# Performance work log

Hardware: AMD Instinct MI355X
Metric: run time of the kernel (lower is better)

## Reference

```python
import jax, jax.numpy as jnp
import numpy as np

TOKEN_SIZE = 4
NEIGHBOR_SIZE = 3


def setup_inputs() -> dict:
    key = jax.random.key(0)
    ks = jax.random.split(key, 8)
    B, C, H, W = 8, 256, 64, 64
    return {
        "blue_feat": jax.random.normal(ks[0], (B, C, H, W), jnp.float32),
        "white_feat": jax.random.normal(ks[1], (B, C, H, W), jnp.float32),
        "Wq": jax.random.normal(ks[2], (C, C), jnp.float32) * 0.05,
        "bq": jax.random.normal(ks[3], (C,), jnp.float32) * 0.05,
        "Wk": jax.random.normal(ks[4], (C, C), jnp.float32) * 0.05,
        "bk": jax.random.normal(ks[5], (C,), jnp.float32) * 0.05,
        "Wv": jax.random.normal(ks[6], (C, C), jnp.float32) * 0.05,
        "bv": jax.random.normal(ks[7], (C,), jnp.float32) * 0.05,
    }


def _tokens(x, nh, nw, ts):
    # [B,C,H,W] -> [B,nh,nw,C,ts*ts]
    B, C = x.shape[0], x.shape[1]
    return (x.reshape(B, C, nh, ts, nw, ts)
             .transpose(0, 2, 4, 1, 3, 5)
             .reshape(B, nh, nw, C, ts * ts))


def reference(blue_feat, white_feat, Wq, bq, Wk, bk, Wv, bv):
    ts, ns = TOKEN_SIZE, NEIGHBOR_SIZE
    pad = ns // 2
    B, C, H, W = blue_feat.shape
    scale = float((ts * ts) ** -0.5)

    # 1x1 conv projections (pointwise channel mix + bias)
    Q = jnp.einsum('bchw,oc->bohw', blue_feat, Wq) + bq[None, :, None, None]
    K = jnp.einsum('bchw,oc->bohw', white_feat, Wk) + bk[None, :, None, None]
    V = jnp.einsum('bchw,oc->bohw', white_feat, Wv) + bv[None, :, None, None]

    nh, nw = H // ts, W // ts  # H,W divisible by ts -> no padding branch
    Qt = _tokens(Q, nh, nw, ts)  # [B,nh,nw,C,D]
    Kt = _tokens(K, nh, nw, ts)
    Vt = _tokens(V, nh, nw, ts)

    # zero-padded token grid, gather 3x3 neighbor tokens (F.unfold equivalent)
    padw = ((0, 0), (pad, pad), (pad, pad), (0, 0), (0, 0))
    Kp = jnp.pad(Kt, padw)
    Vp = jnp.pad(Vt, padw)
    Knb = jnp.stack([Kp[:, di:di + nh, dj:dj + nw]
                     for di in range(ns) for dj in range(ns)], axis=3)  # [B,nh,nw,9,C,D]
    Vnb = jnp.stack([Vp[:, di:di + nh, dj:dj + nw]
                     for di in range(ns) for dj in range(ns)], axis=3)

    # per-channel attention over neighbor tokens
    attn = jax.nn.softmax(
        jnp.einsum('bhwcd,bhwncd->bhwcn', Qt, Knb) * scale, axis=-1)
    out = jnp.einsum('bhwcn,bhwncd->bhwcd', attn, Vnb)  # [B,nh,nw,C,D]

    enhanced = (out.reshape(B, nh, nw, C, ts, ts)
                   .transpose(0, 3, 1, 4, 2, 5)
                   .reshape(B, C, H, W))
    return blue_feat + enhanced  # out_proj is Identity since c1 == c2
```

## Files before the change

kernel.cpp:

```cpp
#include <hip/hip_runtime.h>
#include <hip/hip_bf16.h>
#include <stdint.h>

typedef float  f32x4  __attribute__((ext_vector_type(4)));
typedef float  f32x2  __attribute__((ext_vector_type(2)));
typedef __bf16 bf16x8 __attribute__((ext_vector_type(8)));

#define LROW 40

__global__ __launch_bounds__(256) void wprep_kernel(
    const float* __restrict__ Wq, const float* __restrict__ Wk,
    const float* __restrict__ Wv, __bf16* __restrict__ Wbf)
{
  const int b = blockIdx.x;
  const int t = b >> 5;
  const float* src = (t == 0) ? Wq : (t == 1) ? Wk : Wv;
  const int off = (b & 31) * 2048 + threadIdx.x * 8;
  f32x4 v0 = *(const f32x4*)(src + off);
  f32x4 v1 = *(const f32x4*)(src + off + 4);
  bf16x8 r;
#pragma unroll
  for (int q = 0; q < 4; ++q) { r[q] = (__bf16)v0[q]; r[q + 4] = (__bf16)v1[q]; }
  *(bf16x8*)(Wbf + t * 65536 + off) = r;
}


__global__ __launch_bounds__(256, 3) void proj_gemm3_kernel(
    const float* __restrict__ blue, const float* __restrict__ white,
    const __bf16* __restrict__ Wbf,
    const float* __restrict__ bq, const float* __restrict__ bk,
    const float* __restrict__ bv,
    __bf16* __restrict__ Qt, __bf16* __restrict__ Kt, __bf16* __restrict__ Vt)
{
  __shared__ __bf16 Bs[2][128 * LROW];

  const int bidhw = blockIdx.x;
  const int lid   = (bidhw & 7) * 192 + (bidhw >> 3);
  const int nb    = lid / 6;
  const int bt    = lid % 6;
  const int tensor = (bt < 4) ? 1 + (bt & 1) : 0;
  const int ob     = (bt < 4) ? (bt >> 1) : (bt & 1);

  const float* X    = (tensor == 0) ? blue : white;
  const float* bias = (tensor == 0) ? bq : (tensor == 1) ? bk : bv;
  __bf16*      Out  = (tensor == 0) ? Qt : (tensor == 1) ? Kt : Vt;
  const __bf16* Wp  = Wbf + tensor * 65536 + ob * (128 * 256);

  const int tid  = threadIdx.x;
  const int lane = tid & 63;
  const int wave = tid >> 6;
  const int wo   = wave >> 1;
  const int wn   = wave & 1;

  const int o0    = ob * 128;
  const int n0    = nb * 128;
  const int batch = n0 >> 12;
  const int p0    = n0 & 4095;
  const int tk0   = p0 >> 4;
  const int trow  = tk0 >> 4;
  const int tcol0 = tk0 & 15;
  const float* Xb = X + (size_t)batch * (256 * 4096);

  const int n2   = tid & 63;
  const int ko   = tid >> 6;
  const int nloc = 2 * n2;
  const int tl   = nloc >> 4;
  const int d    = nloc & 15;
  const int hw   = (trow * 4 + (d >> 2)) * 64 + (tcol0 + tl) * 4 + (d & 3);
  const float* srcB0 = Xb + (size_t)(ko * 8) * 4096 + hw;

  const int lrow = lane & 15;
  const int lk   = (lane >> 4) * 8;
  const int aoff = (wo * 64 + lrow) * 256 + lk;

  f32x4 acc[4][4];
#pragma unroll
  for (int i = 0; i < 4; ++i)
#pragma unroll
    for (int j = 0; j < 4; ++j) acc[i][j] = (f32x4)0.0f;

  f32x2 preA[8], preB[8];

#define LOADB(P, kk) { const float* s_ = srcB0 + (size_t)(kk) * 32 * 4096;          \
    P[0] = *(const f32x2*)(s_);         P[1] = *(const f32x2*)(s_ + 4096);          \
    P[2] = *(const f32x2*)(s_ + 8192);  P[3] = *(const f32x2*)(s_ + 12288);         \
    P[4] = *(const f32x2*)(s_ + 16384); P[5] = *(const f32x2*)(s_ + 20480);         \
    P[6] = *(const f32x2*)(s_ + 24576); P[7] = *(const f32x2*)(s_ + 28672); }

#define STEP(P, kk, BUF) {                                                          \
    bf16x8 r0, r1;                                                                  \
    _Pragma("unroll")                                                               \
    for (int t = 0; t < 8; ++t) { r0[t] = (__bf16)P[t][0]; r1[t] = (__bf16)P[t][1]; } \
    *(bf16x8*)(&Bs[BUF][0] + (nloc + 0) * LROW + ko * 8) = r0;                      \
    *(bf16x8*)(&Bs[BUF][0] + (nloc + 1) * LROW + ko * 8) = r1;                      \
    bf16x8 af[4];                                                                   \
    _Pragma("unroll")                                                               \
    for (int i = 0; i < 4; ++i)                                                     \
      af[i] = *(const bf16x8*)(Wp + aoff + i * 4096 + (kk) * 32);                   \
    if ((kk) + 2 < 8) LOADB(P, (kk) + 2);                                           \
    asm volatile("s_waitcnt lgkmcnt(0)" ::: "memory");                              \
    __builtin_amdgcn_s_barrier();                                                   \
    asm volatile("" ::: "memory");                                                  \
    bf16x8 bfrag[4];                                                                \
    _Pragma("unroll")                                                               \
    for (int j = 0; j < 4; ++j)                                                     \
      bfrag[j] = *(const bf16x8*)(&Bs[BUF][0] + (wn * 64 + j * 16 + lrow) * LROW + lk); \
    _Pragma("unroll")                                                               \
    for (int i = 0; i < 4; ++i)                                                     \
      _Pragma("unroll")                                                             \
      for (int j = 0; j < 4; ++j)                                                   \
        acc[i][j] = __builtin_amdgcn_mfma_f32_16x16x32_bf16(af[i], bfrag[j], acc[i][j], 0, 0, 0); \
  }

  LOADB(preA, 0);
  LOADB(preB, 1);

#pragma unroll
  for (int kp = 0; kp < 4; ++kp) {
    STEP(preA, 2 * kp,     0);
    STEP(preB, 2 * kp + 1, 1);
  }
#undef STEP
#undef LOADB

#pragma unroll
  for (int i = 0; i < 4; ++i) {
    const int obase = o0 + wo * 64 + i * 16 + (lane >> 4) * 4;
#pragma unroll
    for (int j = 0; j < 4; ++j) {
      const int n  = n0 + wn * 64 + j * 16 + (lane & 15);
      const int bb = n >> 12;
      const int pp = n & 4095;
      const int tt = pp >> 4;
      const int tii = tt >> 4;
      const int tjj = tt & 15;
      const int dd  = pp & 15;
      const size_t base = ((size_t)(bb * 16 + tii) * 256) * 256 + tjj * 16 + dd;
#pragma unroll
      for (int r = 0; r < 4; ++r) {
        const int o = obase + r;
        const float v = acc[i][j][r] + bias[o];
        Out[base + (size_t)o * 256] = (__bf16)v;
      }
    }
  }
}

__global__ __launch_bounds__(256) void proj_gemm_kernel(
    const float* __restrict__ blue, const float* __restrict__ white,
    const float* __restrict__ Wq, const float* __restrict__ bq,
    const float* __restrict__ Wk, const float* __restrict__ bk,
    const float* __restrict__ Wv, const float* __restrict__ bv,
    __bf16* __restrict__ Qt, __bf16* __restrict__ Kt, __bf16* __restrict__ Vt)
{
  __shared__ __bf16 As[128 * LROW];
  __shared__ __bf16 Bs[128 * LROW];

  const int bidhw = blockIdx.x;
  const int lid   = (bidhw & 7) * 192 + (bidhw >> 3);
  const int nb    = lid / 6;
  const int bt    = lid % 6;
  const int tensor = (bt < 4) ? 1 + (bt & 1) : 0;
  const int ob     = (bt < 4) ? (bt >> 1) : (bt & 1);

  const float* X    = (tensor == 0) ? blue : white;
  const float* W    = (tensor == 0) ? Wq : (tensor == 1) ? Wk : Wv;
  const float* bias = (tensor == 0) ? bq : (tensor == 1) ? bk : bv;
  __bf16*      Out  = (tensor == 0) ? Qt : (tensor == 1) ? Kt : Vt;

  const int tid  = threadIdx.x;
  const int lane = tid & 63;
  const int wave = tid >> 6;
  const int wo   = wave >> 1;
  const int wn   = wave & 1;

  const int o0 = ob * 128;
  const int n0 = nb * 128;
  const int batch = n0 >> 12;
  const int p0    = n0 & 4095;
  const int tk0   = p0 >> 4;
  const int trow  = tk0 >> 4;
  const int tcol0 = tk0 & 15;
  const float* Xb = X + (size_t)batch * (256 * 4096);

  f32x4 acc[4][4];
#pragma unroll
  for (int i = 0; i < 4; ++i)
#pragma unroll
    for (int j = 0; j < 4; ++j) acc[i][j] = (f32x4)0.0f;

  const int arow  = tid >> 1;
  const int ahalf = tid & 1;
  const int n2   = tid & 63;
  const int ko   = tid >> 6;
  const int nloc = 2 * n2;
  const int tl   = nloc >> 4;
  const int d    = nloc & 15;
  const int hw   = (trow * 4 + (d >> 2)) * 64 + (tcol0 + tl) * 4 + (d & 3);

  const int lrow = lane & 15;
  const int lk   = (lane >> 4) * 8;

  for (int kk = 0; kk < 8; ++kk) {
    const int k0 = kk * 32;
    {
      const float* src = W + (size_t)(o0 + arow) * 256 + k0 + ahalf * 16;
      f32x4 t0 = *(const f32x4*)(src + 0);
      f32x4 t1 = *(const f32x4*)(src + 4);
      f32x4 t2 = *(const f32x4*)(src + 8);
      f32x4 t3 = *(const f32x4*)(src + 12);
      bf16x8 c0, c1;
#pragma unroll
      for (int q = 0; q < 4; ++q) { c0[q] = (__bf16)t0[q]; c0[q + 4] = (__bf16)t1[q]; }
#pragma unroll
      for (int q = 0; q < 4; ++q) { c1[q] = (__bf16)t2[q]; c1[q + 4] = (__bf16)t3[q]; }
      __bf16* dst = As + arow * LROW + ahalf * 16;
      *(bf16x8*)(dst + 0) = c0;
      *(bf16x8*)(dst + 8) = c1;
    }
    {
      const float* src = Xb + (size_t)(k0 + ko * 8) * 4096 + hw;
      f32x2 v0 = *(const f32x2*)(src + 0 * 4096);
      f32x2 v1 = *(const f32x2*)(src + 1 * 4096);
      f32x2 v2 = *(const f32x2*)(src + 2 * 4096);
      f32x2 v3 = *(const f32x2*)(src + 3 * 4096);
      f32x2 v4 = *(const f32x2*)(src + 4 * 4096);
      f32x2 v5 = *(const f32x2*)(src + 5 * 4096);
      f32x2 v6 = *(const f32x2*)(src + 6 * 4096);
      f32x2 v7 = *(const f32x2*)(src + 7 * 4096);
      bf16x8 r0, r1;
      r0[0] = (__bf16)v0[0]; r0[1] = (__bf16)v1[0]; r0[2] = (__bf16)v2[0]; r0[3] = (__bf16)v3[0];
      r0[4] = (__bf16)v4[0]; r0[5] = (__bf16)v5[0]; r0[6] = (__bf16)v6[0]; r0[7] = (__bf16)v7[0];
      r1[0] = (__bf16)v0[1]; r1[1] = (__bf16)v1[1]; r1[2] = (__bf16)v2[1]; r1[3] = (__bf16)v3[1];
      r1[4] = (__bf16)v4[1]; r1[5] = (__bf16)v5[1]; r1[6] = (__bf16)v6[1]; r1[7] = (__bf16)v7[1];
      *(bf16x8*)(Bs + (nloc + 0) * LROW + ko * 8) = r0;
      *(bf16x8*)(Bs + (nloc + 1) * LROW + ko * 8) = r1;
    }
    __syncthreads();

    bf16x8 a[4], b[4];
#pragma unroll
    for (int i = 0; i < 4; ++i)
      a[i] = *(const bf16x8*)(As + (wo * 64 + i * 16 + lrow) * LROW + lk);
#pragma unroll
    for (int j = 0; j < 4; ++j)
      b[j] = *(const bf16x8*)(Bs + (wn * 64 + j * 16 + lrow) * LROW + lk);
#pragma unroll
    for (int i = 0; i < 4; ++i)
#pragma unroll
      for (int j = 0; j < 4; ++j)
        acc[i][j] = __builtin_amdgcn_mfma_f32_16x16x32_bf16(a[i], b[j], acc[i][j], 0, 0, 0);
    __syncthreads();
  }

#pragma unroll
  for (int i = 0; i < 4; ++i) {
    const int obase = o0 + wo * 64 + i * 16 + (lane >> 4) * 4;
#pragma unroll
    for (int j = 0; j < 4; ++j) {
      const int n  = n0 + wn * 64 + j * 16 + (lane & 15);
      const int bb = n >> 12;
      const int p  = n & 4095;
      const int tt = p >> 4;
      const int tii = tt >> 4;
      const int tjj = tt & 15;
      const int dd  = p & 15;
      const size_t base = ((size_t)(bb * 16 + tii) * 256) * 256 + tjj * 16 + dd;
#pragma unroll
      for (int r = 0; r < 4; ++r) {
        const int o = obase + r;
        const float v = acc[i][j][r] + bias[o];
        Out[base + (size_t)o * 256] = (__bf16)v;
      }
    }
  }
}

__device__ __forceinline__ void unpack8(const uint4 v, float* f) {
  const uint32_t u0 = v.x, u1 = v.y, u2 = v.z, u3 = v.w;
  f[0] = __uint_as_float(u0 << 16); f[1] = __uint_as_float(u0 & 0xffff0000u);
  f[2] = __uint_as_float(u1 << 16); f[3] = __uint_as_float(u1 & 0xffff0000u);
  f[4] = __uint_as_float(u2 << 16); f[5] = __uint_as_float(u2 & 0xffff0000u);
  f[6] = __uint_as_float(u3 << 16); f[7] = __uint_as_float(u3 & 0xffff0000u);
}

__global__ __launch_bounds__(256) void attn_kernel(
    const __bf16* __restrict__ Qt, const __bf16* __restrict__ Kt,
    const __bf16* __restrict__ Vt, const float* __restrict__ blue,
    float* __restrict__ out)
{
  const int j   = blockIdx.x;
  const int bid = (j & 7) * 256 + (j >> 3);
  const int cg  = bid & 15;
  const int ti  = (bid >> 4) & 15;
  const int b   = bid >> 8;

  const int tid = threadIdx.x;
  const int tj  = tid & 15;
  const int cl  = tid >> 4;
  const int c   = cg * 16 + cl;

  float q[16];
  {
    const __bf16* p = Qt + ((((size_t)b * 16 + ti) * 256 + c) * 16 + tj) * 16;
    unpack8(*(const uint4*)p, q);
    unpack8(*(const uint4*)(p + 8), q + 8);
  }

  float s[9];
#pragma unroll
  for (int n = 0; n < 9; ++n) {
    const int yi = ti + n / 3 - 1;
    const int yj = tj + n % 3 - 1;
    float dot = 0.0f;
    if (yi >= 0 && yi < 16 && yj >= 0 && yj < 16) {
      const __bf16* p = Kt + ((((size_t)b * 16 + yi) * 256 + c) * 16 + yj) * 16;
      float kf[16];
      unpack8(*(const uint4*)p, kf);
      unpack8(*(const uint4*)(p + 8), kf + 8);
#pragma unroll
      for (int dd = 0; dd < 16; ++dd) dot = fmaf(q[dd], kf[dd], dot);
    }
    s[n] = dot * 0.25f;
  }

  float m = s[0];
#pragma unroll
  for (int n = 1; n < 9; ++n) m = fmaxf(m, s[n]);
  float w[9], denom = 0.0f;
#pragma unroll
  for (int n = 0; n < 9; ++n) { w[n] = __expf(s[n] - m); denom += w[n]; }
  const float inv = 1.0f / denom;

  float o16[16];
#pragma unroll
  for (int dd = 0; dd < 16; ++dd) o16[dd] = 0.0f;
#pragma unroll
  for (int n = 0; n < 9; ++n) {
    const int yi = ti + n / 3 - 1;
    const int yj = tj + n % 3 - 1;
    if (yi >= 0 && yi < 16 && yj >= 0 && yj < 16) {
      const __bf16* p = Vt + ((((size_t)b * 16 + yi) * 256 + c) * 16 + yj) * 16;
      float vf[16];
      unpack8(*(const uint4*)p, vf);
      unpack8(*(const uint4*)(p + 8), vf + 8);
#pragma unroll
      for (int dd = 0; dd < 16; ++dd) o16[dd] = fmaf(w[n], vf[dd], o16[dd]);
    }
  }

  const size_t pbase = ((size_t)b * 256 + c) * 4096 + (size_t)(ti * 4) * 64 + tj * 4;
#pragma unroll
  for (int r = 0; r < 4; ++r) {
    f32x4 bl = *(const f32x4*)(blue + pbase + r * 64);
    f32x4 ov;
#pragma unroll
    for (int j2 = 0; j2 < 4; ++j2) ov[j2] = bl[j2] + o16[r * 4 + j2] * inv;
    *(f32x4*)(out + pbase + r * 64) = ov;
  }
}

extern "C" void kernel_launch(void* const* d_in, const int* in_sizes, int n_in,
                              void* d_out, int out_size, void* d_ws, size_t ws_size,
                              hipStream_t stream) {
  const float* blue  = (const float*)d_in[0];
  const float* white = (const float*)d_in[1];
  const float* Wq = (const float*)d_in[2];
  const float* bq = (const float*)d_in[3];
  const float* Wk = (const float*)d_in[4];
  const float* bk = (const float*)d_in[5];
  const float* Wv = (const float*)d_in[6];
  const float* bv = (const float*)d_in[7];
  float* out = (float*)d_out;

  const size_t tsz = (size_t)8 * 256 * 256 * 16;
  __bf16* Qt = (__bf16*)d_ws;
  __bf16* Kt = Qt + tsz;
  __bf16* Vt = Kt + tsz;

  const size_t need = (3 * tsz + 3 * 65536) * sizeof(__bf16);
  if (ws_size >= need) {
    __bf16* Wbf = Vt + tsz;
    wprep_kernel<<<96, 256, 0, stream>>>(Wq, Wk, Wv, Wbf);
    proj_gemm3_kernel<<<1536, 256, 0, stream>>>(blue, white, Wbf, bq, bk, bv, Qt, Kt, Vt);
  } else {
    proj_gemm_kernel<<<1536, 256, 0, stream>>>(blue, white, Wq, bq, Wk, bk, Wv, bv, Qt, Kt, Vt);
  }
  attn_kernel<<<2048, 256, 0, stream>>>(Qt, Kt, Vt, blue, out);
}
```

Before: 81.85 us.

## Triple-buffer projection GEMM LDS with one barrier per k-step and setprio

The projection GEMM moves from a double-buffered LDS scheme to a triple-buffered one. The B tile for the next step is written before the barrier, so each k-step needs only one barrier, and the A fragments are prefetched one step ahead into alternating registers. The LDS row stride drops to 36 with 4-wide stores and loads to change bank-conflict behaviour, and s_setprio is raised around the MFMA block. The costs are more LDS and registers, and the launch-bounds occupancy hint is removed, which may change occupancy.

```diff
diff --git a/kernel.cpp b/kernel.cpp
--- a/kernel.cpp
+++ b/kernel.cpp
@@ -5,17 +5,19 @@
 typedef float  f32x4  __attribute__((ext_vector_type(4)));
 typedef float  f32x2  __attribute__((ext_vector_type(2)));
 typedef __bf16 bf16x8 __attribute__((ext_vector_type(8)));
-
-#define LROW 40
+typedef __bf16 bf16x4 __attribute__((ext_vector_type(4)));
+
+#define LROWF 36
+#define LROW  40
 
 __global__ __launch_bounds__(256) void wprep_kernel(
     const float* __restrict__ Wq, const float* __restrict__ Wk,
     const float* __restrict__ Wv, __bf16* __restrict__ Wbf)
 {
-  const int b = blockIdx.x;
-  const int t = b >> 5;
+  const int wb = blockIdx.x;
+  const int t  = wb >> 5;
   const float* src = (t == 0) ? Wq : (t == 1) ? Wk : Wv;
-  const int off = (b & 31) * 2048 + threadIdx.x * 8;
+  const int off = (wb & 31) * 2048 + threadIdx.x * 8;
   f32x4 v0 = *(const f32x4*)(src + off);
   f32x4 v1 = *(const f32x4*)(src + off + 4);
   bf16x8 r;
@@ -24,33 +26,34 @@
   *(bf16x8*)(Wbf + t * 65536 + off) = r;
 }
 
-
-__global__ __launch_bounds__(256, 3) void proj_gemm3_kernel(
+__global__ __launch_bounds__(256) void gemm_fused_kernel(
     const float* __restrict__ blue, const float* __restrict__ white,
     const __bf16* __restrict__ Wbf,
     const float* __restrict__ bq, const float* __restrict__ bk,
     const float* __restrict__ bv,
     __bf16* __restrict__ Qt, __bf16* __restrict__ Kt, __bf16* __restrict__ Vt)
 {
-  __shared__ __bf16 Bs[2][128 * LROW];
-
-  const int bidhw = blockIdx.x;
-  const int lid   = (bidhw & 7) * 192 + (bidhw >> 3);
-  const int nb    = lid / 6;
-  const int bt    = lid % 6;
+  __shared__ __bf16 Bs[3][128 * LROWF];
+
+  const int bid = blockIdx.x;
+  const int lid = (bid & 7) * 192 + (bid >> 3);
+  const int nb  = lid / 6;
+  const int bt  = lid % 6;
   const int tensor = (bt < 4) ? 1 + (bt & 1) : 0;
   const int ob     = (bt < 4) ? (bt >> 1) : (bt & 1);
 
-  const float* X    = (tensor == 0) ? blue : white;
-  const float* bias = (tensor == 0) ? bq : (tensor == 1) ? bk : bv;
-  __bf16*      Out  = (tensor == 0) ? Qt : (tensor == 1) ? Kt : Vt;
-  const __bf16* Wp  = Wbf + tensor * 65536 + ob * (128 * 256);
+  const float*  X    = (tensor == 0) ? blue : white;
+  const float*  bias = (tensor == 0) ? bq : (tensor == 1) ? bk : bv;
+  __bf16*       Out  = (tensor == 0) ? Qt : (tensor == 1) ? Kt : Vt;
+  const __bf16* Wp   = Wbf + tensor * 65536 + ob * 32768;
 
   const int tid  = threadIdx.x;
   const int lane = tid & 63;
-  const int wave = tid >> 6;
-  const int wo   = wave >> 1;
-  const int wn   = wave & 1;
+  const int w    = tid >> 6;
+  const int wo   = w >> 1;
+  const int wn   = w & 1;
+  const int lrow = lane & 15;
+  const int lks  = lane >> 4;
 
   const int o0    = ob * 128;
   const int n0    = nb * 128;
@@ -67,11 +70,9 @@
   const int tl   = nloc >> 4;
   const int d    = nloc & 15;
   const int hw   = (trow * 4 + (d >> 2)) * 64 + (tcol0 + tl) * 4 + (d & 3);
-  const float* srcB0 = Xb + (size_t)(ko * 8) * 4096 + hw;
-
-  const int lrow = lane & 15;
-  const int lk   = (lane >> 4) * 8;
-  const int aoff = (wo * 64 + lrow) * 256 + lk;
+  const float* srcB = Xb + (size_t)(ko * 8) * 4096 + hw;
+
+  const __bf16* abase = Wp + (size_t)(wo * 64 + lrow) * 256 + lks * 8;
 
   f32x4 acc[4][4];
 #pragma unroll
@@ -79,48 +80,94 @@
 #pragma unroll
     for (int j = 0; j < 4; ++j) acc[i][j] = (f32x4)0.0f;
 
-  f32x2 preA[8], preB[8];
-
-#define LOADB(P, kk) { const float* s_ = srcB0 + (size_t)(kk) * 32 * 4096;          \
-    P[0] = *(const f32x2*)(s_);         P[1] = *(const f32x2*)(s_ + 4096);          \
-    P[2] = *(const f32x2*)(s_ + 8192);  P[3] = *(const f32x2*)(s_ + 12288);         \
-    P[4] = *(const f32x2*)(s_ + 16384); P[5] = *(const f32x2*)(s_ + 20480);         \
-    P[6] = *(const f32x2*)(s_ + 24576); P[7] = *(const f32x2*)(s_ + 28672); }
-
-#define STEP(P, kk, BUF) {                                                          \
-    bf16x8 r0, r1;                                                                  \
-    _Pragma("unroll")                                                               \
-    for (int t = 0; t < 8; ++t) { r0[t] = (__bf16)P[t][0]; r1[t] = (__bf16)P[t][1]; } \
-    *(bf16x8*)(&Bs[BUF][0] + (nloc + 0) * LROW + ko * 8) = r0;                      \
-    *(bf16x8*)(&Bs[BUF][0] + (nloc + 1) * LROW + ko * 8) = r1;                      \
-    bf16x8 af[4];                                                                   \
-    _Pragma("unroll")                                                               \
-    for (int i = 0; i < 4; ++i)                                                     \
-      af[i] = *(const bf16x8*)(Wp + aoff + i * 4096 + (kk) * 32);                   \
-    if ((kk) + 2 < 8) LOADB(P, (kk) + 2);                                           \
-    asm volatile("s_waitcnt lgkmcnt(0)" ::: "memory");                              \
-    __builtin_amdgcn_s_barrier();                                                   \
-    asm volatile("" ::: "memory");                                                  \
-    bf16x8 bfrag[4];                                                                \
-    _Pragma("unroll")                                                               \
-    for (int j = 0; j < 4; ++j)                                                     \
-      bfrag[j] = *(const bf16x8*)(&Bs[BUF][0] + (wn * 64 + j * 16 + lrow) * LROW + lk); \
-    _Pragma("unroll")                                                               \
-    for (int i = 0; i < 4; ++i)                                                     \
-      _Pragma("unroll")                                                             \
-      for (int j = 0; j < 4; ++j)                                                   \
-        acc[i][j] = __builtin_amdgcn_mfma_f32_16x16x32_bf16(af[i], bfrag[j], acc[i][j], 0, 0, 0); \
-  }
-
-  LOADB(preA, 0);
-  LOADB(preB, 1);
-
-#pragma unroll
-  for (int kp = 0; kp < 4; ++kp) {
-    STEP(preA, 2 * kp,     0);
-    STEP(preB, 2 * kp + 1, 1);
-  }
-#undef STEP
+  f32x2  pA[8], pB[8];
+  bf16x8 afA[4], afB[4];
+
+#define LOADB(P, kk) do { const float* s_ = srcB + (size_t)(kk) * 32 * 4096;   \
+    P[0] = *(const f32x2*)(s_);         P[1] = *(const f32x2*)(s_ + 4096);     \
+    P[2] = *(const f32x2*)(s_ + 8192);  P[3] = *(const f32x2*)(s_ + 12288);    \
+    P[4] = *(const f32x2*)(s_ + 16384); P[5] = *(const f32x2*)(s_ + 20480);    \
+    P[6] = *(const f32x2*)(s_ + 24576); P[7] = *(const f32x2*)(s_ + 28672);    \
+  } while (0)
+
+#define LOADA(AF, kk) do {                                                     \
+    _Pragma("unroll")                                                          \
+    for (int i = 0; i < 4; ++i)                                                \
+      AF[i] = *(const bf16x8*)(abase + (size_t)i * 16 * 256 + (kk) * 32);      \
+  } while (0)
+
+#define WRITEB(P, BUF) do {                                                    \
+    __bf16* bp = &Bs[BUF][nloc * LROWF + ko * 8];                              \
+    bf16x4 a0, a1, b0, b1;                                                     \
+    a0[0] = (__bf16)P[0][0]; a0[1] = (__bf16)P[1][0];                          \
+    a0[2] = (__bf16)P[2][0]; a0[3] = (__bf16)P[3][0];                          \
+    a1[0] = (__bf16)P[4][0]; a1[1] = (__bf16)P[5][0];                          \
+    a1[2] = (__bf16)P[6][0]; a1[3] = (__bf16)P[7][0];                          \
+    b0[0] = (__bf16)P[0][1]; b0[1] = (__bf16)P[1][1];                          \
+    b0[2] = (__bf16)P[2][1]; b0[3] = (__bf16)P[3][1];                          \
+    b1[0] = (__bf16)P[4][1]; b1[1] = (__bf16)P[5][1];                          \
+    b1[2] = (__bf16)P[6][1]; b1[3] = (__bf16)P[7][1];                          \
+    *(bf16x4*)(bp)             = a0;  *(bf16x4*)(bp + 4)         = a1;         \
+    *(bf16x4*)(bp + LROWF)     = b0;  *(bf16x4*)(bp + LROWF + 4) = b1;         \
+  } while (0)
+
+#define COMPUTE(BUF, AF) do {                                                  \
+    bf16x8 bfr[4];                                                             \
+    _Pragma("unroll")                                                          \
+    for (int j = 0; j < 4; ++j) {                                              \
+      const int row = wn * 64 + j * 16 + lrow;                                 \
+      bf16x4 x0 = *(const bf16x4*)&Bs[BUF][row * LROWF + lks * 8];             \
+      bf16x4 x1 = *(const bf16x4*)&Bs[BUF][row * LROWF + lks * 8 + 4];         \
+      bf16x8 v;                                                                \
+      v[0] = x0[0]; v[1] = x0[1]; v[2] = x0[2]; v[3] = x0[3];                  \
+      v[4] = x1[0]; v[5] = x1[1]; v[6] = x1[2]; v[7] = x1[3];                  \
+      bfr[j] = v;                                                              \
+    }                                                                          \
+    __builtin_amdgcn_s_setprio(1);                                             \
+    _Pragma("unroll")                                                          \
+    for (int i = 0; i < 4; ++i)                                                \
+      _Pragma("unroll")                                                        \
+      for (int j = 0; j < 4; ++j)                                              \
+        acc[i][j] = __builtin_amdgcn_mfma_f32_16x16x32_bf16(AF[i], bfr[j],     \
+                                                            acc[i][j], 0, 0, 0);\
+    __builtin_amdgcn_s_setprio(0);                                             \
+  } while (0)
+
+#define BAR() do {                                                             \
+    asm volatile("s_waitcnt lgkmcnt(0)" ::: "memory");                         \
+    __builtin_amdgcn_sched_barrier(0);                                         \
+    __builtin_amdgcn_s_barrier();                                              \
+    __builtin_amdgcn_sched_barrier(0);                                         \
+  } while (0)
+
+  LOADB(pA, 0);
+  LOADB(pB, 1);
+  LOADA(afA, 0);
+  WRITEB(pA, 0);
+  LOADB(pA, 2);
+  BAR();
+
+#define BODY(T, PW, AFN, AFC) do {                                             \
+    if ((T) < 7) LOADA(AFN, (T) + 1);                                          \
+    if ((T) < 7) WRITEB(PW, ((T) + 1) % 3);                                    \
+    if ((T) < 5) LOADB(PW, (T) + 3);                                           \
+    BAR();                                                                     \
+    COMPUTE((T) % 3, AFC);                                                     \
+  } while (0)
+
+  BODY(0, pB, afB, afA);
+  BODY(1, pA, afA, afB);
+  BODY(2, pB, afB, afA);
+  BODY(3, pA, afA, afB);
+  BODY(4, pB, afB, afA);
+  BODY(5, pA, afA, afB);
+  BODY(6, pB, afB, afA);
+  BODY(7, pA, afA, afB);
+#undef BODY
+#undef BAR
+#undef COMPUTE
+#undef WRITEB
+#undef LOADA
 #undef LOADB
 
 #pragma unroll
@@ -211,9 +258,9 @@
       f32x4 t3 = *(const f32x4*)(src + 12);
       bf16x8 c0, c1;
 #pragma unroll
-      for (int q = 0; q < 4; ++q) { c0[q] = (__bf16)t0[q]; c0[q + 4] = (__bf16)t1[q]; }
-#pragma unroll
-      for (int q = 0; q < 4; ++q) { c1[q] = (__bf16)t2[q]; c1[q + 4] = (__bf16)t3[q]; }
+      for (int qq = 0; qq < 4; ++qq) { c0[qq] = (__bf16)t0[qq]; c0[qq + 4] = (__bf16)t1[qq]; }
+#pragma unroll
+      for (int qq = 0; qq < 4; ++qq) { c1[qq] = (__bf16)t2[qq]; c1[qq + 4] = (__bf16)t3[qq]; }
       __bf16* dst = As + arow * LROW + ahalf * 16;
       *(bf16x8*)(dst + 0) = c0;
       *(bf16x8*)(dst + 8) = c1;
@@ -382,7 +429,7 @@
   if (ws_size >= need) {
     __bf16* Wbf = Vt + tsz;
     wprep_kernel<<<96, 256, 0, stream>>>(Wq, Wk, Wv, Wbf);
-    proj_gemm3_kernel<<<1536, 256, 0, stream>>>(blue, white, Wbf, bq, bk, bv, Qt, Kt, Vt);
+    gemm_fused_kernel<<<1536, 256, 0, stream>>>(blue, white, Wbf, bq, bk, bv, Qt, Kt, Vt);
   } else {
     proj_gemm_kernel<<<1536, 256, 0, stream>>>(blue, white, Wq, bq, Wk, bk, Wv, bv, Qt, Kt, Vt);
   }
```

Result: no change. 82.65 us (+1.0%).
